# Kernel tuning notes

Hardware: AMD Instinct MI355X
Metric: run time of the kernel (lower is better)

## Reference

```python
import jax, jax.numpy as jnp
import numpy as np

# Image grid matching params nImgX/nImgY; nImgZ == nDctY (slice-wise 2D parallel-beam BP)
NIMG_X = 512
NIMG_Y = 512


def _backproject(proj):
    """Pixel-driven 2D parallel-beam backprojection applied per slice.

    proj: (nView, Z, nDct) sinogram (views over [0, pi), unit detector/pixel spacing,
    detector and image both centered). Returns vol: (Z, NIMG_Y, NIMG_X),
    scaled by pi/nView (the weighting the original module applies, cf. its backward).
    """
    nView, Z, nDct = proj.shape
    thetas = jnp.arange(nView, dtype=jnp.float32) * (np.pi / nView)
    xs = jnp.arange(NIMG_X, dtype=jnp.float32) - (NIMG_X - 1) / 2.0
    ys = jnp.arange(NIMG_Y, dtype=jnp.float32) - (NIMG_Y - 1) / 2.0
    ctr = (nDct - 1) / 2.0

    def step(vol, inp):
        p, c, s = inp                      # p: (Z, nDct)
        t = xs[None, :] * c + ys[:, None] * s + ctr   # (Y, X) detector coordinate
        i0 = jnp.floor(t).astype(jnp.int32)
        w = t - i0.astype(jnp.float32)
        v0 = (i0 >= 0) & (i0 < nDct)
        v1 = ((i0 + 1) >= 0) & ((i0 + 1) < nDct)
        i0c = jnp.clip(i0, 0, nDct - 1)
        i1c = jnp.clip(i0 + 1, 0, nDct - 1)
        g0 = p[:, i0c]                      # (Z, Y, X) gather
        g1 = p[:, i1c]
        contrib = g0 * jnp.where(v0, 1.0 - w, 0.0)[None] + g1 * jnp.where(v1, w, 0.0)[None]
        return vol + contrib, None

    vol0 = jnp.zeros((Z, NIMG_Y, NIMG_X), dtype=proj.dtype)
    vol, _ = jax.lax.scan(step, vol0, (proj, jnp.cos(thetas), jnp.sin(thetas)))
    return vol * jnp.float32(np.pi / nView)


def setup_inputs() -> dict:
    key = jax.random.key(0)
    # sinogram: (nDctY=32 slices, 1, nView=720, nDctX=1024)
    x = jax.random.normal(key, (32, 1, 720, 1024), dtype=jnp.float32)
    return {"x": x}


def reference(x):
    # original: squeeze -> (Z, nView, nDct) -> transpose(1,0,2) -> (nView, Z, nDct)
    proj = jnp.transpose(x[:, 0], (1, 0, 2))
    vol = _backproject(proj)               # (Z, NIMG_Y, NIMG_X)
    return vol[:, None, :, :]              # (nImgZ, 1, nImgY, nImgX)
```

## Files before the change

kernel.cpp:

```cpp
#include <hip/hip_runtime.h>
#include <math.h>

#define NVIEW 720
#define NDCT  1024
#define NZ    32
#define NX    512
#define NY    512

#define BX 16
#define BY 16
#define ZG 16
#define NR 24
#define RSTRIDE 20

typedef unsigned int uint;

#if __has_builtin(__builtin_amdgcn_fdot2)
#define USE_FDOT2 1
typedef _Float16 half2v __attribute__((ext_vector_type(2)));
#else
#define USE_FDOT2 0
#endif

__device__ __forceinline__ uint f2bf_rne(float f) {
    uint u = __float_as_uint(f);
    return (u + 0x7fffu + ((u >> 16) & 1u)) >> 16;
}

__device__ __forceinline__ uint pack_word(float a, float b) {
#if USE_FDOT2
    union { _Float16 h[2]; uint u; } r;
    r.h[0] = (_Float16)a;
    r.h[1] = (_Float16)(b - a);
    return r.u;
#else
    uint lo = f2bf_rne(b - a);
    uint u  = (f2bf_rne(a) << 16) | lo;
    uint up = u + 0x10000u, um = u - 0x10000u;
    float e0 = fabsf(__uint_as_float(u)  - a);
    float e1 = fabsf(__uint_as_float(up) - a);
    float e2 = fabsf(__uint_as_float(um) - a);
    if (e1 < e0) { u = up; e0 = e1; }
    if (e2 < e0) { u = um; }
    return u;
#endif
}

__global__ __launch_bounds__(64) void pack_kernel(const float* __restrict__ x,
                                                  uint* __restrict__ packed) {
    __shared__ uint tr[64 * 33];
    const int l  = threadIdx.x;
    const int v  = blockIdx.x;
    const int ib = blockIdx.y * 64;
    const bool last = (ib + 64 >= NDCT);
    const float* rowbase = x + (size_t)v * NDCT + ib;

    float pre = 0.0f;
    if (l < NZ && !last) pre = rowbase[(size_t)l * (NVIEW * NDCT) + 64];

    for (int z = 0; z < NZ; ++z) {
        const float* r = rowbase + (size_t)z * (NVIEW * NDCT);
        float a   = r[l];
        float a64 = __shfl(pre, z);
        float b   = __shfl(a, l + 1);
        if (l == 63) b = a64;
        tr[l * 33 + z] = pack_word(a, b);
    }
    __syncthreads();

    uint* obase = packed + ((size_t)v * NDCT + ib) * 32;
    #pragma unroll
    for (int it = 0; it < 8; ++it) {
        int c  = it * 64 + l;
        int il = c >> 3;
        int zc = (c & 7) * 4;
        uint4 w4;
        w4.x = tr[il * 33 + zc + 0];
        w4.y = tr[il * 33 + zc + 1];
        w4.z = tr[il * 33 + zc + 2];
        w4.w = tr[il * 33 + zc + 3];
        *(uint4*)(obase + (size_t)c * 4) = w4;
    }
}

#if USE_FDOT2
#define SAMPLE(zz, uu) do { \
    union { uint q; half2v h; } _c; _c.q = (uu); \
    acc[zz] = __builtin_amdgcn_fdot2(_c.h, wpair, acc[zz], false); \
} while (0)
#else
#define SAMPLE(zz, uu) do { \
    acc[zz] += __uint_as_float(uu); \
    acc[zz]  = fmaf(w, __uint_as_float((uu) << 16), acc[zz]); \
} while (0)
#endif

__global__ __launch_bounds__(256, 8) void bp_lds(const uint* __restrict__ packed,
                                                 float* __restrict__ out) {
    __shared__ float2 cs[NVIEW];
    __shared__ int imintab[NVIEW];
    __shared__ __align__(16) uint stage[2][NR * RSTRIDE];

    const int tid = threadIdx.y * BX + threadIdx.x;
    const int g   = blockIdx.z;
    const float xf0 = (float)(int)(blockIdx.x * BX) - 255.5f;
    const float yf0 = (float)(int)(blockIdx.y * BY) - 255.5f;

    for (int v = tid; v < NVIEW; v += BX * BY) {
        float th = (float)v * (float)(M_PI / NVIEW);
        float s, c;
        sincosf(th, &s, &c);
        cs[v] = make_float2(c, s);
        float b0 = fmaf(yf0, s, 511.5f);
        float b1 = fmaf(yf0 + (float)(BY - 1), s, 511.5f);
        float t00 = fmaf(xf0, c, b0);
        float t10 = fmaf(xf0 + (float)(BX - 1), c, b0);
        float t01 = fmaf(xf0, c, b1);
        float t11 = fmaf(xf0 + (float)(BX - 1), c, b1);
        imintab[v] = (int)fminf(fminf(t00, t10), fminf(t01, t11));
    }
    __syncthreads();

    const int x = blockIdx.x * BX + threadIdx.x;
    const int y = blockIdx.y * BY + threadIdx.y;
    const float xf = (float)x - 255.5f;
    const float yf = (float)y - 255.5f;

    float acc[ZG];
    #pragma unroll
    for (int z = 0; z < ZG; ++z) acc[z] = 0.0f;

    const int  wv   = tid >> 6;
    const int  ln   = tid & 63;
    const bool sact = (ln < 24);
    const int  slot = wv * 24 + ln;
    const int  sr   = slot >> 2;
    const int  sch  = slot & 3;
    const size_t sg_off = ((size_t)sr << 5) + (g << 4) + (sch << 2);
    const int  swr  = sr * RSTRIDE + (sch << 2);

    uint4 st;
    if (sact) {
        st = *(const uint4*)(packed + ((size_t)imintab[0] << 5) + sg_off);
        *(uint4*)&stage[0][swr] = st;
    }
    __syncthreads();

    #pragma unroll 2
    for (int v = 0; v < NVIEW; ++v) {
        if (sact && v + 1 < NVIEW) {
            st = *(const uint4*)(packed + ((size_t)(v + 1) << 15)
                                 + ((size_t)imintab[v + 1] << 5) + sg_off);
        }

        float2 a = cs[v];
        float t  = fmaf(xf, a.x, fmaf(yf, a.y, 511.5f));
        int   i0 = (int)t;
        float w  = t - (float)i0;
        int   rl = i0 - imintab[v];

#if USE_FDOT2
        half2v wpair;
        wpair[0] = (_Float16)1.0f;
        wpair[1] = (_Float16)w;
#endif

        const uint* sp = stage[v & 1] + rl * RSTRIDE;
        uint4 q0 = *(const uint4*)(sp);
        uint4 q1 = *(const uint4*)(sp + 4);
        uint4 q2 = *(const uint4*)(sp + 8);
        uint4 q3 = *(const uint4*)(sp + 12);

        SAMPLE( 0, q0.x); SAMPLE( 1, q0.y); SAMPLE( 2, q0.z); SAMPLE( 3, q0.w);
        SAMPLE( 4, q1.x); SAMPLE( 5, q1.y); SAMPLE( 6, q1.z); SAMPLE( 7, q1.w);
        SAMPLE( 8, q2.x); SAMPLE( 9, q2.y); SAMPLE(10, q2.z); SAMPLE(11, q2.w);
        SAMPLE(12, q3.x); SAMPLE(13, q3.y); SAMPLE(14, q3.z); SAMPLE(15, q3.w);

        if (sact && v + 1 < NVIEW) *(uint4*)&stage[(v + 1) & 1][swr] = st;
        __syncthreads();
    }

    const float scale = 0.0043633231299858236f;
    #pragma unroll
    for (int lz = 0; lz < ZG; ++lz) {
        out[(((size_t)(g * ZG + lz)) * NY + y) * NX + x] = acc[lz] * scale;
    }
}

__global__ __launch_bounds__(256) void bp_direct(const float* __restrict__ xin,
                                                 float* __restrict__ out) {
    __shared__ float2 cs[NVIEW];
    int lt = threadIdx.y * 64 + threadIdx.x;
    for (int v = lt; v < NVIEW; v += 256) {
        float th = (float)v * (float)(M_PI / NVIEW);
        float s, c;
        sincosf(th, &s, &c);
        cs[v] = make_float2(c, s);
    }
    __syncthreads();

    int x = blockIdx.x * 64 + threadIdx.x;
    int y = blockIdx.y * 4 + threadIdx.y;
    float xf = (float)x - 255.5f;
    float yf = (float)y - 255.5f;

    float acc[NZ];
    #pragma unroll
    for (int z = 0; z < NZ; ++z) acc[z] = 0.0f;

    for (int v = 0; v < NVIEW; ++v) {
        float2 a = cs[v];
        float t  = fmaf(xf, a.x, fmaf(yf, a.y, 511.5f));
        int   i0 = (int)t;
        float w  = t - (float)i0;
        const float* p = xin + (size_t)v * NDCT + i0;
        #pragma unroll
        for (int z = 0; z < NZ; ++z) {
            float g0 = p[(size_t)z * NVIEW * NDCT];
            float g1 = p[(size_t)z * NVIEW * NDCT + 1];
            acc[z] += fmaf(w, g1 - g0, g0);
        }
    }

    const float scale = 0.0043633231299858236f;
    #pragma unroll
    for (int z = 0; z < NZ; ++z) {
        out[((size_t)z * NY + y) * NX + x] = acc[z] * scale;
    }
}

extern "C" void kernel_launch(void* const* d_in, const int* in_sizes, int n_in,
                              void* d_out, int out_size, void* d_ws, size_t ws_size,
                              hipStream_t stream) {
    const float* x = (const float*)d_in[0];
    float* out = (float*)d_out;

    const size_t packed_bytes = (size_t)NVIEW * NDCT * NZ * sizeof(uint);

    if (ws_size >= packed_bytes) {
        uint* packed = (uint*)d_ws;
        pack_kernel<<<dim3(NVIEW, NDCT / 64), 64, 0, stream>>>(x, packed);
        bp_lds<<<dim3(NX / BX, NY / BY, 2), dim3(BX, BY), 0, stream>>>(packed, out);
    } else {
        bp_direct<<<dim3(NX / 64, NY / 4), dim3(64, 4), 0, stream>>>(x, out);
    }
}
```

Measured before the change: 666.6 us.

## Compute two adjacent pixels per thread and fold view table into float4

Each thread now handles two horizontally adjacent pixels with 16 z accumulators each, so the block shrinks to 128 threads and the per-view setup (table read, coordinate math, barrier) is amortized over twice the work. The per-view cos, sin, offset and imin are packed into one float4 table entry, and the first pixel's detector index is computed directly relative to the staged window. The second pixel reuses the first pixel's LDS rows when both fall on the same detector bin, skipping a second set of LDS loads. Output stores become float2. The cost is more registers per thread, a data-dependent branch, and fewer threads per block for latency hiding.

```diff
diff --git a/kernel.cpp b/kernel.cpp
--- a/kernel.cpp
+++ b/kernel.cpp
@@ -7,9 +7,6 @@
 #define NX    512
 #define NY    512
 
-#define BX 16
-#define BY 16
-#define ZG 16
 #define NR 24
 #define RSTRIDE 20
 
@@ -84,106 +81,131 @@
 }
 
 #if USE_FDOT2
-#define SAMPLE(zz, uu) do { \
+#define SAMP(A, zz, uu, WP, WF) do { \
     union { uint q; half2v h; } _c; _c.q = (uu); \
-    acc[zz] = __builtin_amdgcn_fdot2(_c.h, wpair, acc[zz], false); \
+    A[zz] = __builtin_amdgcn_fdot2(_c.h, (WP), A[zz], false); \
 } while (0)
 #else
-#define SAMPLE(zz, uu) do { \
-    acc[zz] += __uint_as_float(uu); \
-    acc[zz]  = fmaf(w, __uint_as_float((uu) << 16), acc[zz]); \
+#define SAMP(A, zz, uu, WP, WF) do { \
+    A[zz] += __uint_as_float(uu); \
+    A[zz]  = fmaf((WF), __uint_as_float((uu) << 16), A[zz]); \
 } while (0)
 #endif
 
-__global__ __launch_bounds__(256, 8) void bp_lds(const uint* __restrict__ packed,
+#define SAMPLE16(A, WP, WF) do { \
+    SAMP(A, 0, q0.x, WP, WF); SAMP(A, 1, q0.y, WP, WF); \
+    SAMP(A, 2, q0.z, WP, WF); SAMP(A, 3, q0.w, WP, WF); \
+    SAMP(A, 4, q1.x, WP, WF); SAMP(A, 5, q1.y, WP, WF); \
+    SAMP(A, 6, q1.z, WP, WF); SAMP(A, 7, q1.w, WP, WF); \
+    SAMP(A, 8, q2.x, WP, WF); SAMP(A, 9, q2.y, WP, WF); \
+    SAMP(A,10, q2.z, WP, WF); SAMP(A,11, q2.w, WP, WF); \
+    SAMP(A,12, q3.x, WP, WF); SAMP(A,13, q3.y, WP, WF); \
+    SAMP(A,14, q3.z, WP, WF); SAMP(A,15, q3.w, WP, WF); \
+} while (0)
+
+__global__ __launch_bounds__(128, 4) void bp_lds(const uint* __restrict__ packed,
                                                  float* __restrict__ out) {
-    __shared__ float2 cs[NVIEW];
-    __shared__ int imintab[NVIEW];
+    __shared__ float4 tab[NVIEW];
     __shared__ __align__(16) uint stage[2][NR * RSTRIDE];
 
-    const int tid = threadIdx.y * BX + threadIdx.x;
+    const int tid = threadIdx.y * 8 + threadIdx.x;
     const int g   = blockIdx.z;
-    const float xf0 = (float)(int)(blockIdx.x * BX) - 255.5f;
-    const float yf0 = (float)(int)(blockIdx.y * BY) - 255.5f;
-
-    for (int v = tid; v < NVIEW; v += BX * BY) {
+    const float xf0 = (float)(int)(blockIdx.x * 16) - 255.5f;
+    const float yf0 = (float)(int)(blockIdx.y * 16) - 255.5f;
+
+    for (int v = tid; v < NVIEW; v += 128) {
         float th = (float)v * (float)(M_PI / NVIEW);
         float s, c;
         sincosf(th, &s, &c);
-        cs[v] = make_float2(c, s);
         float b0 = fmaf(yf0, s, 511.5f);
-        float b1 = fmaf(yf0 + (float)(BY - 1), s, 511.5f);
+        float b1 = fmaf(yf0 + 15.0f, s, 511.5f);
         float t00 = fmaf(xf0, c, b0);
-        float t10 = fmaf(xf0 + (float)(BX - 1), c, b0);
+        float t10 = fmaf(xf0 + 15.0f, c, b0);
         float t01 = fmaf(xf0, c, b1);
-        float t11 = fmaf(xf0 + (float)(BX - 1), c, b1);
-        imintab[v] = (int)fminf(fminf(t00, t10), fminf(t01, t11));
-    }
-    __syncthreads();
-
-    const int x = blockIdx.x * BX + threadIdx.x;
-    const int y = blockIdx.y * BY + threadIdx.y;
-    const float xf = (float)x - 255.5f;
-    const float yf = (float)y - 255.5f;
-
-    float acc[ZG];
-    #pragma unroll
-    for (int z = 0; z < ZG; ++z) acc[z] = 0.0f;
+        float t11 = fmaf(xf0 + 15.0f, c, b1);
+        int imin = (int)fminf(fminf(t00, t10), fminf(t01, t11));
+        tab[v] = make_float4(c, s, 511.5f - (float)imin, __int_as_float(imin));
+    }
+    __syncthreads();
+
+    const int x0 = blockIdx.x * 16 + threadIdx.x * 2;
+    const int y  = blockIdx.y * 16 + threadIdx.y;
+    const float xf = (float)x0 - 255.5f;
+    const float yf = (float)y  - 255.5f;
+
+    float acc0[16], acc1[16];
+    #pragma unroll
+    for (int z = 0; z < 16; ++z) { acc0[z] = 0.0f; acc1[z] = 0.0f; }
 
     const int  wv   = tid >> 6;
     const int  ln   = tid & 63;
-    const bool sact = (ln < 24);
-    const int  slot = wv * 24 + ln;
+    const bool sact = (ln < 48);
+    const int  slot = wv * 48 + ln;
     const int  sr   = slot >> 2;
     const int  sch  = slot & 3;
     const size_t sg_off = ((size_t)sr << 5) + (g << 4) + (sch << 2);
     const int  swr  = sr * RSTRIDE + (sch << 2);
 
+    float4 t4 = tab[0];
     uint4 st;
     if (sact) {
-        st = *(const uint4*)(packed + ((size_t)imintab[0] << 5) + sg_off);
+        st = *(const uint4*)(packed + ((size_t)__float_as_int(t4.w) << 5) + sg_off);
         *(uint4*)&stage[0][swr] = st;
     }
     __syncthreads();
 
     #pragma unroll 2
     for (int v = 0; v < NVIEW; ++v) {
+        float4 t4n = t4;
+        if (v + 1 < NVIEW) t4n = tab[v + 1];
         if (sact && v + 1 < NVIEW) {
             st = *(const uint4*)(packed + ((size_t)(v + 1) << 15)
-                                 + ((size_t)imintab[v + 1] << 5) + sg_off);
+                                 + ((size_t)__float_as_int(t4n.w) << 5) + sg_off);
         }
 
-        float2 a = cs[v];
-        float t  = fmaf(xf, a.x, fmaf(yf, a.y, 511.5f));
-        int   i0 = (int)t;
-        float w  = t - (float)i0;
-        int   rl = i0 - imintab[v];
+        const float c = t4.x;
+        float t0 = fmaf(xf, c, fmaf(yf, t4.y, t4.z));
+        float t1 = t0 + c;
+        int   i0 = (int)t0;
+        int   i1 = (int)t1;
+        float w0 = t0 - (float)i0;
+        float w1 = t1 - (float)i1;
 
 #if USE_FDOT2
-        half2v wpair;
-        wpair[0] = (_Float16)1.0f;
-        wpair[1] = (_Float16)w;
-#endif
-
-        const uint* sp = stage[v & 1] + rl * RSTRIDE;
+        half2v wp0; wp0[0] = (_Float16)1.0f; wp0[1] = (_Float16)w0;
+        half2v wp1; wp1[0] = (_Float16)1.0f; wp1[1] = (_Float16)w1;
+#else
+        const int wp0 = 0, wp1 = 0;
+#endif
+
+        const uint* sp = stage[v & 1] + i0 * RSTRIDE;
         uint4 q0 = *(const uint4*)(sp);
         uint4 q1 = *(const uint4*)(sp + 4);
         uint4 q2 = *(const uint4*)(sp + 8);
         uint4 q3 = *(const uint4*)(sp + 12);
 
-        SAMPLE( 0, q0.x); SAMPLE( 1, q0.y); SAMPLE( 2, q0.z); SAMPLE( 3, q0.w);
-        SAMPLE( 4, q1.x); SAMPLE( 5, q1.y); SAMPLE( 6, q1.z); SAMPLE( 7, q1.w);
-        SAMPLE( 8, q2.x); SAMPLE( 9, q2.y); SAMPLE(10, q2.z); SAMPLE(11, q2.w);
-        SAMPLE(12, q3.x); SAMPLE(13, q3.y); SAMPLE(14, q3.z); SAMPLE(15, q3.w);
+        SAMPLE16(acc0, wp0, w0);
+
+        if (i1 != i0) {
+            const uint* sp1 = stage[v & 1] + i1 * RSTRIDE;
+            q0 = *(const uint4*)(sp1);
+            q1 = *(const uint4*)(sp1 + 4);
+            q2 = *(const uint4*)(sp1 + 8);
+            q3 = *(const uint4*)(sp1 + 12);
+        }
+
+        SAMPLE16(acc1, wp1, w1);
 
         if (sact && v + 1 < NVIEW) *(uint4*)&stage[(v + 1) & 1][swr] = st;
         __syncthreads();
+        t4 = t4n;
     }
 
     const float scale = 0.0043633231299858236f;
     #pragma unroll
-    for (int lz = 0; lz < ZG; ++lz) {
-        out[(((size_t)(g * ZG + lz)) * NY + y) * NX + x] = acc[lz] * scale;
+    for (int lz = 0; lz < 16; ++lz) {
+        float2 o = make_float2(acc0[lz] * scale, acc1[lz] * scale);
+        *(float2*)(out + (((size_t)(g * 16 + lz)) * NY + y) * NX + x0) = o;
     }
 }
 
@@ -240,7 +262,7 @@
     if (ws_size >= packed_bytes) {
         uint* packed = (uint*)d_ws;
         pack_kernel<<<dim3(NVIEW, NDCT / 64), 64, 0, stream>>>(x, packed);
-        bp_lds<<<dim3(NX / BX, NY / BY, 2), dim3(BX, BY), 0, stream>>>(packed, out);
+        bp_lds<<<dim3(NX / 16, NY / 16, 2), dim3(8, 16), 0, stream>>>(packed, out);
     } else {
         bp_direct<<<dim3(NX / 64, NY / 4), dim3(64, 4), 0, stream>>>(x, out);
     }
```

After: 629.4 us. -5.6%, faster.
